# Optimization experiments

Measured on AMD Instinct MI355X. Metric: run time of the kernel, lower is better.

Reference implementation:

```python
import jax, jax.numpy as jnp
import numpy as np

B, T, H, E, D, K = 4, 4096, 2048, 8, 1024, 2

def setup_inputs() -> dict:
    key = jax.random.key(0)
    ks = jax.random.split(key, 7)
    x  = jax.random.normal(ks[0], (B, T, H), dtype=jnp.float32)
    Wr = jax.random.normal(ks[1], (H, E), dtype=jnp.float32) * (1.0 / np.sqrt(H))
    br = jnp.zeros((E,), dtype=jnp.float32)
    We = jax.random.normal(ks[2], (E, H, D), dtype=jnp.float32) * (1.0 / np.sqrt(H))
    be = jnp.zeros((E, D), dtype=jnp.float32)
    Wc = jax.random.normal(ks[3], (D, H), dtype=jnp.float32) * (1.0 / np.sqrt(D))
    bc = jnp.zeros((H,), dtype=jnp.float32)
    return {"x": x, "Wr": Wr, "br": br, "We": We, "be": be, "Wc": Wc, "bc": bc}

def reference(x, Wr, br, We, be, Wc, bc):
    # Router: [B,T,H] @ [H,E] -> [B,T,E]
    router_logits = jnp.einsum('bth,he->bte', x, Wr) + br
    scores = jax.nn.softmax(router_logits, axis=-1)
    # top-k over experts (sorted descending, like torch.topk)
    topk_scores, topk_idx = jax.lax.top_k(scores, K)  # [B,T,K]
    # Dense all-expert linear: [B,T,E,D]
    expert_outs = jnp.einsum('bth,ehd->bted', x, We) + be
    # Gather the chosen experts per token: [B,T,K,D]
    gather_idx = jnp.broadcast_to(topk_idx[..., None], (B, T, K, D))
    chosen = jnp.take_along_axis(expert_outs, gather_idx, axis=2)
    # Weighted sum over top-k: [B,T,D]
    weighted = jnp.sum(chosen * topk_scores[..., None], axis=2)
    # Combine: [B,T,D] @ [D,H] -> [B,T,H]
    return jnp.einsum('btd,dh->bth', weighted, Wc) + bc
```

## Files before the change

kernel.cpp:

```cpp
#include <hip/hip_runtime.h>
#include <hip/hip_bf16.h>

typedef float f32x4 __attribute__((ext_vector_type(4)));
typedef short bf16x8 __attribute__((ext_vector_type(8)));

#define M_NT 16
#define M_OFF 17
#define M_TBL 32
#define MAX_TILES 264
#define NCHUNK 1024

__device__ __forceinline__ void gload16(const void* g, void* l) {
  __builtin_amdgcn_global_load_lds(
      (const __attribute__((address_space(1))) void*)g,
      (__attribute__((address_space(3))) void*)l, 16, 0, 0);
}

__device__ __forceinline__ float bf2f(unsigned short u) {
  union { unsigned int i; float f; } v; v.i = ((unsigned int)u) << 16; return v.f;
}
__device__ __forceinline__ unsigned short f2bf(float f) {
  __hip_bfloat16 h = __float2bfloat16(f);
  return __builtin_bit_cast(unsigned short, h);
}

__global__ void transpose_cvt(const float* __restrict__ src,
                              unsigned short* __restrict__ dst, int R, int C) {
  __shared__ float tile[32][33];
  int b = blockIdx.z;
  int c0 = blockIdx.x * 32, r0 = blockIdx.y * 32;
  src += (size_t)b * R * C;
  dst += (size_t)b * R * C;
  int tx = threadIdx.x, ty = threadIdx.y;
#pragma unroll
  for (int i = 0; i < 32; i += 8)
    tile[ty + i][tx] = src[(size_t)(r0 + ty + i) * C + c0 + tx];
  __syncthreads();
#pragma unroll
  for (int i = 0; i < 32; i += 8)
    dst[(size_t)(c0 + ty + i) * R + r0 + tx] = f2bf(tile[tx][ty + i]);
}

__global__ __launch_bounds__(256) void router_kernel(
    const float* __restrict__ x, const float* __restrict__ Wr,
    const float* __restrict__ br, unsigned short* __restrict__ xbf,
    float* __restrict__ scores, int* __restrict__ idx,
    int* __restrict__ blk_hist) {
  __shared__ int cnt[8];
  int tid = threadIdx.x, lane = tid & 63, w = tid >> 6;
  if (tid < 8) cnt[tid] = 0;
  __syncthreads();
  int t0 = blockIdx.x * 16 + w * 4;
  const float* xr = x + (size_t)t0 * 2048;
  unsigned short* xo = xbf + (size_t)t0 * 2048;
  float acc[4][8] = {};
#pragma unroll
  for (int j = 0; j < 8; ++j) {
    int h0 = j * 256 + lane * 4;
    float4 xv[4];
#pragma unroll
    for (int t = 0; t < 4; ++t) xv[t] = *(const float4*)(xr + (size_t)t * 2048 + h0);
#pragma unroll
    for (int t = 0; t < 4; ++t) {
      ushort4 p;
      p.x = f2bf(xv[t].x); p.y = f2bf(xv[t].y);
      p.z = f2bf(xv[t].z); p.w = f2bf(xv[t].w);
      *(ushort4*)(xo + (size_t)t * 2048 + h0) = p;
    }
    const float4* wp = (const float4*)(Wr + (size_t)h0 * 8);
#pragma unroll
    for (int c = 0; c < 4; ++c) {
      float4 w0 = wp[2 * c], w1 = wp[2 * c + 1];
      float xc0 = (c == 0) ? xv[0].x : (c == 1) ? xv[0].y : (c == 2) ? xv[0].z : xv[0].w;
      float xc1 = (c == 0) ? xv[1].x : (c == 1) ? xv[1].y : (c == 2) ? xv[1].z : xv[1].w;
      float xc2 = (c == 0) ? xv[2].x : (c == 1) ? xv[2].y : (c == 2) ? xv[2].z : xv[2].w;
      float xc3 = (c == 0) ? xv[3].x : (c == 1) ? xv[3].y : (c == 2) ? xv[3].z : xv[3].w;
      acc[0][0] += xc0 * w0.x; acc[0][1] += xc0 * w0.y; acc[0][2] += xc0 * w0.z; acc[0][3] += xc0 * w0.w;
      acc[0][4] += xc0 * w1.x; acc[0][5] += xc0 * w1.y; acc[0][6] += xc0 * w1.z; acc[0][7] += xc0 * w1.w;
      acc[1][0] += xc1 * w0.x; acc[1][1] += xc1 * w0.y; acc[1][2] += xc1 * w0.z; acc[1][3] += xc1 * w0.w;
      acc[1][4] += xc1 * w1.x; acc[1][5] += xc1 * w1.y; acc[1][6] += xc1 * w1.z; acc[1][7] += xc1 * w1.w;
      acc[2][0] += xc2 * w0.x; acc[2][1] += xc2 * w0.y; acc[2][2] += xc2 * w0.z; acc[2][3] += xc2 * w0.w;
      acc[2][4] += xc2 * w1.x; acc[2][5] += xc2 * w1.y; acc[2][6] += xc2 * w1.z; acc[2][7] += xc2 * w1.w;
      acc[3][0] += xc3 * w0.x; acc[3][1] += xc3 * w0.y; acc[3][2] += xc3 * w0.z; acc[3][3] += xc3 * w0.w;
      acc[3][4] += xc3 * w1.x; acc[3][5] += xc3 * w1.y; acc[3][6] += xc3 * w1.z; acc[3][7] += xc3 * w1.w;
    }
  }
#pragma unroll
  for (int t = 0; t < 4; ++t)
#pragma unroll
    for (int e = 0; e < 8; ++e)
#pragma unroll
      for (int off = 32; off > 0; off >>= 1)
        acc[t][e] += __shfl_xor(acc[t][e], off);
  if (lane < 4) {
    int t = t0 + lane;
    float l[8];
#pragma unroll
    for (int e = 0; e < 8; ++e) {
      float v = (lane == 0) ? acc[0][e] : (lane == 1) ? acc[1][e]
              : (lane == 2) ? acc[2][e] : acc[3][e];
      l[e] = v + br[e];
    }
    float mx = l[0];
#pragma unroll
    for (int e = 1; e < 8; ++e) mx = fmaxf(mx, l[e]);
    float se = 0.f;
#pragma unroll
    for (int e = 0; e < 8; ++e) se += __expf(l[e] - mx);
    float inv = 1.f / se;
    int e1 = 0; float b1 = l[0];
#pragma unroll
    for (int e = 1; e < 8; ++e) if (l[e] > b1) { b1 = l[e]; e1 = e; }
    int e2 = -1; float b2 = -1e30f;
#pragma unroll
    for (int e = 0; e < 8; ++e) if (e != e1 && l[e] > b2) { b2 = l[e]; e2 = e; }
    idx[2 * t] = e1; idx[2 * t + 1] = e2;
    scores[2 * t] = __expf(b1 - mx) * inv;
    scores[2 * t + 1] = __expf(b2 - mx) * inv;
    atomicAdd(&cnt[e1], 1);
    atomicAdd(&cnt[e2], 1);
  }
  __syncthreads();
  if (tid < 8) blk_hist[blockIdx.x * 8 + tid] = cnt[tid];
}

__global__ __launch_bounds__(512) void scan_kernel(
    const int* __restrict__ blk_hist, int* __restrict__ chunk_base,
    int* __restrict__ meta, int* __restrict__ rowlist) {
  __shared__ int stot[8], soff[8];
  int tid = threadIdx.x, lane = tid & 63, e = tid >> 6;
  int running = 0;
  for (int g = 0; g < NCHUNK / 64; ++g) {
    int c = g * 64 + lane;
    int v = blk_hist[c * 8 + e];
    int orig = v;
#pragma unroll
    for (int off = 1; off < 64; off <<= 1) {
      int n = __shfl_up(v, off);
      if (lane >= off) v += n;
    }
    chunk_base[c * 8 + e] = running + v - orig;
    running += __shfl(v, 63);
  }
  if (lane == 0) stot[e] = running;
  __syncthreads();
  if (tid == 0) {
    int off = 0, nt = 0;
    int4* tbl = (int4*)(meta + M_TBL);
    for (int ee = 0; ee < 8; ++ee) {
      int c = stot[ee];
      meta[M_OFF + ee] = off; soff[ee] = off;
      int tiles = (c + 127) >> 7;
      for (int t = 0; t < tiles; ++t)
        tbl[nt++] = make_int4(ee, off + t * 128, min(128, c - t * 128), 0);
      off += tiles << 7;
    }
    meta[M_NT] = nt;
  }
  __syncthreads();
  for (int ee = 0; ee < 8; ++ee) {
    int c = stot[ee], end = ((c + 127) >> 7) << 7;
    for (int i = c + tid; i < end; i += 512) rowlist[soff[ee] + i] = 0;
  }
}

__global__ void scatter_kernel(const int* __restrict__ idx,
                               const int* __restrict__ chunk_base,
                               const int* __restrict__ meta,
                               int* __restrict__ rowlist) {
  int c = blockIdx.x, lane = threadIdx.x;
  int entry = c * 32 + lane;
  int e = (lane < 32) ? idx[entry] : -1;
#pragma unroll
  for (int ee = 0; ee < 8; ++ee) {
    unsigned long long m = __ballot(e == ee);
    if (e == ee) {
      int rank = __popcll(m & ((1ull << lane) - 1));
      rowlist[meta[M_OFF + ee] + chunk_base[c * 8 + ee] + rank] = entry;
    }
  }
}

__global__ __launch_bounds__(256) void expert_gemm(
    const unsigned short* __restrict__ xbf,
    const unsigned short* __restrict__ WeT,
    const float* __restrict__ be,
    const float* __restrict__ scores,
    const int* __restrict__ rowlist,
    const int* __restrict__ meta,
    unsigned short* __restrict__ z) {
  __shared__ short lA[128 * 32];
  __shared__ short lB[128 * 32];
  __shared__ int lrows[128];
  if ((int)blockIdx.y >= meta[M_NT]) return;
  int4 tt = ((const int4*)(meta + M_TBL))[blockIdx.y];
  int e = tt.x, base = tt.y, valid = tt.z;
  int n0 = blockIdx.x * 128;
  int tid = threadIdx.x, lane = tid & 63, w = tid >> 6;
  if (tid < 128) lrows[tid] = rowlist[base + tid];
  __syncthreads();
  int ch0 = 2 * w, ch1 = ch0 + 1;
  int sub = lane >> 2, colb = (lane & 3) * 8;
  int ra0 = lrows[ch0 * 16 + sub] >> 1;
  int ra1 = lrows[ch1 * 16 + sub] >> 1;
  const unsigned short* sA0 = xbf + (size_t)ra0 * 2048 + colb;
  const unsigned short* sA1 = xbf + (size_t)ra1 * 2048 + colb;
  const unsigned short* Bb = WeT + (size_t)e * 1024 * 2048;
  const unsigned short* sB0 = Bb + (size_t)(n0 + ch0 * 16 + sub) * 2048 + colb;
  const unsigned short* sB1 = Bb + (size_t)(n0 + ch1 * 16 + sub) * 2048 + colb;
  f32x4 acc[4][4] = {};
  int wr = (w >> 1) * 64, wc = (w & 1) * 64;
  int fl = lane & 15, q = lane >> 4;
  for (int k0 = 0; k0 < 2048; k0 += 32) {
    __syncthreads();
    gload16(sA0, lA + ch0 * 512);
    gload16(sA1, lA + ch1 * 512);
    gload16(sB0, lB + ch0 * 512);
    gload16(sB1, lB + ch1 * 512);
    sA0 += 32; sA1 += 32; sB0 += 32; sB1 += 32;
    __syncthreads();
    bf16x8 a[4], b[4];
#pragma unroll
    for (int i = 0; i < 4; ++i) a[i] = *(const bf16x8*)(lA + (wr + i * 16 + fl) * 32 + q * 8);
#pragma unroll
    for (int i = 0; i < 4; ++i) b[i] = *(const bf16x8*)(lB + (wc + i * 16 + fl) * 32 + q * 8);
#pragma unroll
    for (int mi = 0; mi < 4; ++mi)
#pragma unroll
      for (int ni = 0; ni < 4; ++ni)
        acc[mi][ni] = __builtin_amdgcn_mfma_f32_16x16x32_bf16(a[mi], b[ni], acc[mi][ni], 0, 0, 0);
  }
  float bev[4];
#pragma unroll
  for (int ni = 0; ni < 4; ++ni) bev[ni] = be[e * 1024 + n0 + wc + ni * 16 + fl];
#pragma unroll
  for (int mi = 0; mi < 4; ++mi)
#pragma unroll
    for (int r = 0; r < 4; ++r) {
      int row = wr + mi * 16 + q * 4 + r;
      if (row < valid) {
        int entry = lrows[row];
        float s = scores[entry];
        unsigned short* zr = z + (size_t)entry * 1024 + n0 + wc;
#pragma unroll
        for (int ni = 0; ni < 4; ++ni)
          zr[ni * 16 + fl] = f2bf((acc[mi][ni][r] + bev[ni]) * s);
      }
    }
}

__global__ void wsum_kernel(const unsigned short* __restrict__ z,
                            unsigned short* __restrict__ y) {
  size_t i = ((size_t)blockIdx.x * 256 + threadIdx.x) * 8;
  size_t t = i >> 10, d = i & 1023;
  int4 za = *(const int4*)(z + (t * 2) * 1024 + d);
  int4 zb = *(const int4*)(z + (t * 2 + 1) * 1024 + d);
  int4 r;
  const unsigned short* pa = (const unsigned short*)&za;
  const unsigned short* pb = (const unsigned short*)&zb;
  unsigned short* pr = (unsigned short*)&r;
#pragma unroll
  for (int j = 0; j < 8; ++j) pr[j] = f2bf(bf2f(pa[j]) + bf2f(pb[j]));
  *(int4*)(y + i) = r;
}

__global__ __launch_bounds__(256) void combine_gemm(
    const unsigned short* __restrict__ y,
    const unsigned short* __restrict__ WcT,
    const float* __restrict__ bc,
    float* __restrict__ out) {
  __shared__ short lA[128 * 32];
  __shared__ short lB[128 * 32];
  int tid = threadIdx.x, lane = tid & 63, w = tid >> 6;
  int m0 = blockIdx.y * 128, n0 = blockIdx.x * 128;
  int ch0 = 2 * w, ch1 = ch0 + 1;
  int sub = lane >> 2, colb = (lane & 3) * 8;
  const unsigned short* sA0 = y + (size_t)(m0 + ch0 * 16 + sub) * 1024 + colb;
  const unsigned short* sA1 = y + (size_t)(m0 + ch1 * 16 + sub) * 1024 + colb;
  const unsigned short* sB0 = WcT + (size_t)(n0 + ch0 * 16 + sub) * 1024 + colb;
  const unsigned short* sB1 = WcT + (size_t)(n0 + ch1 * 16 + sub) * 1024 + colb;
  f32x4 acc[4][4] = {};
  int wr = (w >> 1) * 64, wc = (w & 1) * 64;
  int fl = lane & 15, q = lane >> 4;
  for (int k0 = 0; k0 < 1024; k0 += 32) {
    __syncthreads();
    gload16(sA0, lA + ch0 * 512);
    gload16(sA1, lA + ch1 * 512);
    gload16(sB0, lB + ch0 * 512);
    gload16(sB1, lB + ch1 * 512);
    sA0 += 32; sA1 += 32; sB0 += 32; sB1 += 32;
    __syncthreads();
    bf16x8 a[4], b[4];
#pragma unroll
    for (int i = 0; i < 4; ++i) a[i] = *(const bf16x8*)(lA + (wr + i * 16 + fl) * 32 + q * 8);
#pragma unroll
    for (int i = 0; i < 4; ++i) b[i] = *(const bf16x8*)(lB + (wc + i * 16 + fl) * 32 + q * 8);
#pragma unroll
    for (int mi = 0; mi < 4; ++mi)
#pragma unroll
      for (int ni = 0; ni < 4; ++ni)
        acc[mi][ni] = __builtin_amdgcn_mfma_f32_16x16x32_bf16(a[mi], b[ni], acc[mi][ni], 0, 0, 0);
  }
  float bcv[4];
#pragma unroll
  for (int ni = 0; ni < 4; ++ni) bcv[ni] = bc[n0 + wc + ni * 16 + fl];
#pragma unroll
  for (int mi = 0; mi < 4; ++mi)
#pragma unroll
    for (int r = 0; r < 4; ++r) {
      int row = m0 + wr + mi * 16 + q * 4 + r;
      float* orow = out + (size_t)row * 2048 + n0 + wc;
#pragma unroll
      for (int ni = 0; ni < 4; ++ni) orow[ni * 16 + fl] = acc[mi][ni][r] + bcv[ni];
    }
}

extern "C" void kernel_launch(void* const* d_in, const int* in_sizes, int n_in,
                              void* d_out, int out_size, void* d_ws, size_t ws_size,
                              hipStream_t stream) {
  const float* x  = (const float*)d_in[0];
  const float* Wr = (const float*)d_in[1];
  const float* br = (const float*)d_in[2];
  const float* We = (const float*)d_in[3];
  const float* be = (const float*)d_in[4];
  const float* Wc = (const float*)d_in[5];
  const float* bc = (const float*)d_in[6];
  float* out = (float*)d_out;

  char* ws = (char*)d_ws;
  size_t o = 0;
  auto alloc = [&](size_t b) {
    char* p = ws + o;
    o = (o + b + 255) & ~(size_t)255;
    return p;
  };
  unsigned short* xbf = (unsigned short*)alloc(16384UL * 2048 * 2);
  unsigned short* WeT = (unsigned short*)alloc(8UL * 1024 * 2048 * 2);
  unsigned short* WcT = (unsigned short*)alloc(2048UL * 1024 * 2);
  unsigned short* z   = (unsigned short*)alloc(32768UL * 1024 * 2);
  unsigned short* yw  = (unsigned short*)alloc(16384UL * 1024 * 2);
  float* scores = (float*)alloc(32768UL * 4);
  int* idx      = (int*)alloc(32768UL * 4);
  int* rowlist  = (int*)alloc(33792UL * 4);
  int* meta     = (int*)alloc(8192);
  int* blk_hist = (int*)alloc(NCHUNK * 8 * 4);
  int* chunk_base = (int*)alloc(NCHUNK * 8 * 4);
  (void)ws_size; (void)in_sizes; (void)n_in; (void)out_size;

  hipLaunchKernelGGL(transpose_cvt, dim3(32, 64, 8), dim3(32, 8), 0, stream, We, WeT, 2048, 1024);
  hipLaunchKernelGGL(transpose_cvt, dim3(64, 32, 1), dim3(32, 8), 0, stream, Wc, WcT, 1024, 2048);
  hipLaunchKernelGGL(router_kernel, dim3(NCHUNK), dim3(256), 0, stream, x, Wr, br, xbf, scores, idx, blk_hist);
  hipLaunchKernelGGL(scan_kernel, dim3(1), dim3(512), 0, stream, blk_hist, chunk_base, meta, rowlist);
  hipLaunchKernelGGL(scatter_kernel, dim3(NCHUNK), dim3(64), 0, stream, idx, chunk_base, meta, rowlist);
  hipLaunchKernelGGL(expert_gemm, dim3(8, MAX_TILES), dim3(256), 0, stream,
                     xbf, WeT, be, scores, rowlist, meta, z);
  hipLaunchKernelGGL(wsum_kernel, dim3(8192), dim3(256), 0, stream, z, yw);
  hipLaunchKernelGGL(combine_gemm, dim3(16, 128), dim3(256), 0, stream, yw, WcT, bc, out);
}
```

Measured before the change: 433.0 us.

## Use 256x256 double-buffered swizzled LDS tiles for expert and combine GEMMs

Both GEMMs move from 128x128 tiles with a 32-wide K step and a load-then-sync loop to 256x256 tiles run by 512-thread blocks. Each K step is now 64 wide, with XOR-swizzled LDS layout and two LDS buffers: the next tile is fetched asynchronously while the current one is used, and waits are coordinated with explicit vmcnt counts. Block indices are remapped to group work for better cache locality, and the router scan now pads each expert to 256 rows instead of 128. The intent is more data reuse per LDS load and overlap of memory with MFMA work. The tradeoff is heavy register pressure from 128 accumulator floats per thread under a two-blocks-per-CU launch bound, and 128KB of shared memory per block, which limits occupancy.

```diff
diff --git a/kernel.cpp b/kernel.cpp
--- a/kernel.cpp
+++ b/kernel.cpp
@@ -7,7 +7,7 @@
 #define M_NT 16
 #define M_OFF 17
 #define M_TBL 32
-#define MAX_TILES 264
+#define MAX_TILES 136
 #define NCHUNK 1024
 
 __device__ __forceinline__ void gload16(const void* g, void* l) {
@@ -150,16 +150,16 @@
     for (int ee = 0; ee < 8; ++ee) {
       int c = stot[ee];
       meta[M_OFF + ee] = off; soff[ee] = off;
-      int tiles = (c + 127) >> 7;
+      int tiles = (c + 255) >> 8;
       for (int t = 0; t < tiles; ++t)
-        tbl[nt++] = make_int4(ee, off + t * 128, min(128, c - t * 128), 0);
-      off += tiles << 7;
+        tbl[nt++] = make_int4(ee, off + t * 256, min(256, c - t * 256), 0);
+      off += tiles << 8;
     }
     meta[M_NT] = nt;
   }
   __syncthreads();
   for (int ee = 0; ee < 8; ++ee) {
-    int c = stot[ee], end = ((c + 127) >> 7) << 7;
+    int c = stot[ee], end = ((c + 255) >> 8) << 8;
     for (int i = c + tid; i < end; i += 512) rowlist[soff[ee] + i] = 0;
   }
 }
@@ -181,7 +181,8 @@
   }
 }
 
-__global__ __launch_bounds__(256) void expert_gemm(
+
+__global__ __launch_bounds__(512, 2) void expert_gemm(
     const unsigned short* __restrict__ xbf,
     const unsigned short* __restrict__ WeT,
     const float* __restrict__ be,
@@ -189,64 +190,216 @@
     const int* __restrict__ rowlist,
     const int* __restrict__ meta,
     unsigned short* __restrict__ z) {
-  __shared__ short lA[128 * 32];
-  __shared__ short lB[128 * 32];
-  __shared__ int lrows[128];
-  if ((int)blockIdx.y >= meta[M_NT]) return;
-  int4 tt = ((const int4*)(meta + M_TBL))[blockIdx.y];
+  __shared__ char smem[131072];
+  __shared__ int lrows[256];
+  int nt = meta[M_NT];
+  int flat = blockIdx.y * 4 + blockIdx.x;
+  int work = (flat & 7) * 68 + (flat >> 3);
+  int tileid = work >> 2, nb = work & 3;
+  if (tileid >= nt) return;
+  int4 tt = ((const int4*)(meta + M_TBL))[tileid];
   int e = tt.x, base = tt.y, valid = tt.z;
-  int n0 = blockIdx.x * 128;
+  int n0 = nb * 256;
   int tid = threadIdx.x, lane = tid & 63, w = tid >> 6;
-  if (tid < 128) lrows[tid] = rowlist[base + tid];
-  __syncthreads();
-  int ch0 = 2 * w, ch1 = ch0 + 1;
-  int sub = lane >> 2, colb = (lane & 3) * 8;
-  int ra0 = lrows[ch0 * 16 + sub] >> 1;
-  int ra1 = lrows[ch1 * 16 + sub] >> 1;
-  const unsigned short* sA0 = xbf + (size_t)ra0 * 2048 + colb;
-  const unsigned short* sA1 = xbf + (size_t)ra1 * 2048 + colb;
-  const unsigned short* Bb = WeT + (size_t)e * 1024 * 2048;
-  const unsigned short* sB0 = Bb + (size_t)(n0 + ch0 * 16 + sub) * 2048 + colb;
-  const unsigned short* sB1 = Bb + (size_t)(n0 + ch1 * 16 + sub) * 2048 + colb;
-  f32x4 acc[4][4] = {};
-  int wr = (w >> 1) * 64, wc = (w & 1) * 64;
+  if (tid < 256) lrows[tid] = rowlist[base + tid];
+  __syncthreads();
+  int rsub = lane >> 3;
+  int slot = ((lane & 7) ^ rsub) * 16;
+  const char* pa[4]; const char* pb[4];
+#pragma unroll
+  for (int j = 0; j < 4; ++j) {
+    int r = w * 32 + j * 8 + rsub;
+    int tok = lrows[r] >> 1;
+    pa[j] = (const char*)(xbf + (size_t)tok * 2048) + slot;
+    pb[j] = (const char*)WeT + ((size_t)e * 1024 + n0 + r) * 4096 + slot;
+  }
+#pragma unroll
+  for (int t2 = 0; t2 < 2; ++t2) {
+    char* da = smem + t2 * 32768 + w * 4096;
+    char* db = smem + 65536 + t2 * 32768 + w * 4096;
+#pragma unroll
+    for (int j = 0; j < 4; ++j) { gload16(pa[j], da + j * 1024); pa[j] += 128; }
+#pragma unroll
+    for (int j = 0; j < 4; ++j) { gload16(pb[j], db + j * 1024); pb[j] += 128; }
+  }
+  __builtin_amdgcn_sched_barrier(0);
+  f32x4 acc[8][4] = {};
+  int wm = w >> 2, wn = w & 3;
   int fl = lane & 15, q = lane >> 4;
-  for (int k0 = 0; k0 < 2048; k0 += 32) {
-    __syncthreads();
-    gload16(sA0, lA + ch0 * 512);
-    gload16(sA1, lA + ch1 * 512);
-    gload16(sB0, lB + ch0 * 512);
-    gload16(sB1, lB + ch1 * 512);
-    sA0 += 32; sA1 += 32; sB0 += 32; sB1 += 32;
-    __syncthreads();
-    bf16x8 a[4], b[4];
-#pragma unroll
-    for (int i = 0; i < 4; ++i) a[i] = *(const bf16x8*)(lA + (wr + i * 16 + fl) * 32 + q * 8);
-#pragma unroll
-    for (int i = 0; i < 4; ++i) b[i] = *(const bf16x8*)(lB + (wc + i * 16 + fl) * 32 + q * 8);
-#pragma unroll
-    for (int mi = 0; mi < 4; ++mi)
-#pragma unroll
-      for (int ni = 0; ni < 4; ++ni)
-        acc[mi][ni] = __builtin_amdgcn_mfma_f32_16x16x32_bf16(a[mi], b[ni], acc[mi][ni], 0, 0, 0);
+  int swz = (fl & 7) << 4;
+  const int NT2 = 32;
+  for (int t = 0; t < NT2; ++t) {
+    if (t + 1 < NT2) { asm volatile("s_waitcnt vmcnt(8)" ::: "memory"); }
+    else             { asm volatile("s_waitcnt vmcnt(0)" ::: "memory"); }
+    __builtin_amdgcn_sched_barrier(0);
+    __builtin_amdgcn_s_barrier();
+    __builtin_amdgcn_sched_barrier(0);
+    const char* Ab = smem + (t & 1) * 32768;
+    const char* Bb = smem + 65536 + (t & 1) * 32768;
+#pragma unroll
+    for (int mh = 0; mh < 2; ++mh)
+#pragma unroll
+      for (int nh = 0; nh < 2; ++nh) {
+        bf16x8 av[4][2], bv[2][2];
+#pragma unroll
+        for (int m = 0; m < 4; ++m)
+#pragma unroll
+          for (int kk = 0; kk < 2; ++kk) {
+            int row = wm * 128 + mh * 64 + m * 16 + fl;
+            av[m][kk] = *(const bf16x8*)(Ab + row * 128 + ((kk * 64 + q * 16) ^ swz));
+          }
+#pragma unroll
+        for (int n = 0; n < 2; ++n)
+#pragma unroll
+          for (int kk = 0; kk < 2; ++kk) {
+            int row = wn * 64 + nh * 32 + n * 16 + fl;
+            bv[n][kk] = *(const bf16x8*)(Bb + row * 128 + ((kk * 64 + q * 16) ^ swz));
+          }
+        __builtin_amdgcn_s_setprio(1);
+#pragma unroll
+        for (int m = 0; m < 4; ++m)
+#pragma unroll
+          for (int n = 0; n < 2; ++n)
+#pragma unroll
+            for (int kk = 0; kk < 2; ++kk)
+              acc[mh * 4 + m][nh * 2 + n] = __builtin_amdgcn_mfma_f32_16x16x32_bf16(
+                  av[m][kk], bv[n][kk], acc[mh * 4 + m][nh * 2 + n], 0, 0, 0);
+        __builtin_amdgcn_s_setprio(0);
+      }
+    __builtin_amdgcn_sched_barrier(0);
+    __builtin_amdgcn_s_barrier();
+    __builtin_amdgcn_sched_barrier(0);
+    if (t + 2 < NT2) {
+      char* da = smem + (t & 1) * 32768 + w * 4096;
+      char* db = smem + 65536 + (t & 1) * 32768 + w * 4096;
+#pragma unroll
+      for (int j = 0; j < 4; ++j) { gload16(pa[j], da + j * 1024); pa[j] += 128; }
+#pragma unroll
+      for (int j = 0; j < 4; ++j) { gload16(pb[j], db + j * 1024); pb[j] += 128; }
+    }
   }
   float bev[4];
 #pragma unroll
-  for (int ni = 0; ni < 4; ++ni) bev[ni] = be[e * 1024 + n0 + wc + ni * 16 + fl];
-#pragma unroll
-  for (int mi = 0; mi < 4; ++mi)
+  for (int nc = 0; nc < 4; ++nc)
+    bev[nc] = be[e * 1024 + n0 + wn * 64 + (nc >> 1) * 32 + (nc & 1) * 16 + fl];
+#pragma unroll
+  for (int mi = 0; mi < 8; ++mi) {
+    int rowbase = wm * 128 + (mi >> 2) * 64 + (mi & 3) * 16 + q * 4;
 #pragma unroll
     for (int r = 0; r < 4; ++r) {
-      int row = wr + mi * 16 + q * 4 + r;
+      int row = rowbase + r;
       if (row < valid) {
         int entry = lrows[row];
         float s = scores[entry];
-        unsigned short* zr = z + (size_t)entry * 1024 + n0 + wc;
-#pragma unroll
-        for (int ni = 0; ni < 4; ++ni)
-          zr[ni * 16 + fl] = f2bf((acc[mi][ni][r] + bev[ni]) * s);
+        unsigned short* zr = z + (size_t)entry * 1024 + n0 + wn * 64 + fl;
+#pragma unroll
+        for (int nc = 0; nc < 4; ++nc)
+          zr[(nc >> 1) * 32 + (nc & 1) * 16] = f2bf((acc[mi][nc][r] + bev[nc]) * s);
       }
     }
+  }
+}
+
+__global__ __launch_bounds__(512, 2) void combine_gemm(
+    const unsigned short* __restrict__ y,
+    const unsigned short* __restrict__ WcT,
+    const float* __restrict__ bc,
+    float* __restrict__ out) {
+  __shared__ char smem[131072];
+  int flat = blockIdx.y * 8 + blockIdx.x;
+  int work = (flat & 7) * 64 + (flat >> 3);
+  int mtile = work >> 3, nb = work & 7;
+  int m0 = mtile * 256, n0 = nb * 256;
+  int tid = threadIdx.x, lane = tid & 63, w = tid >> 6;
+  int rsub = lane >> 3;
+  int slot = ((lane & 7) ^ rsub) * 16;
+  const char* pa[4]; const char* pb[4];
+#pragma unroll
+  for (int j = 0; j < 4; ++j) {
+    int r = w * 32 + j * 8 + rsub;
+    pa[j] = (const char*)y + (size_t)(m0 + r) * 2048 + slot;
+    pb[j] = (const char*)WcT + (size_t)(n0 + r) * 2048 + slot;
+  }
+#pragma unroll
+  for (int t2 = 0; t2 < 2; ++t2) {
+    char* da = smem + t2 * 32768 + w * 4096;
+    char* db = smem + 65536 + t2 * 32768 + w * 4096;
+#pragma unroll
+    for (int j = 0; j < 4; ++j) { gload16(pa[j], da + j * 1024); pa[j] += 128; }
+#pragma unroll
+    for (int j = 0; j < 4; ++j) { gload16(pb[j], db + j * 1024); pb[j] += 128; }
+  }
+  __builtin_amdgcn_sched_barrier(0);
+  f32x4 acc[8][4] = {};
+  int wm = w >> 2, wn = w & 3;
+  int fl = lane & 15, q = lane >> 4;
+  int swz = (fl & 7) << 4;
+  const int NT2 = 16;
+  for (int t = 0; t < NT2; ++t) {
+    if (t + 1 < NT2) { asm volatile("s_waitcnt vmcnt(8)" ::: "memory"); }
+    else             { asm volatile("s_waitcnt vmcnt(0)" ::: "memory"); }
+    __builtin_amdgcn_sched_barrier(0);
+    __builtin_amdgcn_s_barrier();
+    __builtin_amdgcn_sched_barrier(0);
+    const char* Ab = smem + (t & 1) * 32768;
+    const char* Bb = smem + 65536 + (t & 1) * 32768;
+#pragma unroll
+    for (int mh = 0; mh < 2; ++mh)
+#pragma unroll
+      for (int nh = 0; nh < 2; ++nh) {
+        bf16x8 av[4][2], bv[2][2];
+#pragma unroll
+        for (int m = 0; m < 4; ++m)
+#pragma unroll
+          for (int kk = 0; kk < 2; ++kk) {
+            int row = wm * 128 + mh * 64 + m * 16 + fl;
+            av[m][kk] = *(const bf16x8*)(Ab + row * 128 + ((kk * 64 + q * 16) ^ swz));
+          }
+#pragma unroll
+        for (int n = 0; n < 2; ++n)
+#pragma unroll
+          for (int kk = 0; kk < 2; ++kk) {
+            int row = wn * 64 + nh * 32 + n * 16 + fl;
+            bv[n][kk] = *(const bf16x8*)(Bb + row * 128 + ((kk * 64 + q * 16) ^ swz));
+          }
+        __builtin_amdgcn_s_setprio(1);
+#pragma unroll
+        for (int m = 0; m < 4; ++m)
+#pragma unroll
+          for (int n = 0; n < 2; ++n)
+#pragma unroll
+            for (int kk = 0; kk < 2; ++kk)
+              acc[mh * 4 + m][nh * 2 + n] = __builtin_amdgcn_mfma_f32_16x16x32_bf16(
+                  av[m][kk], bv[n][kk], acc[mh * 4 + m][nh * 2 + n], 0, 0, 0);
+        __builtin_amdgcn_s_setprio(0);
+      }
+    __builtin_amdgcn_sched_barrier(0);
+    __builtin_amdgcn_s_barrier();
+    __builtin_amdgcn_sched_barrier(0);
+    if (t + 2 < NT2) {
+      char* da = smem + (t & 1) * 32768 + w * 4096;
+      char* db = smem + 65536 + (t & 1) * 32768 + w * 4096;
+#pragma unroll
+      for (int j = 0; j < 4; ++j) { gload16(pa[j], da + j * 1024); pa[j] += 128; }
+#pragma unroll
+      for (int j = 0; j < 4; ++j) { gload16(pb[j], db + j * 1024); pb[j] += 128; }
+    }
+  }
+  float bcv[4];
+#pragma unroll
+  for (int nc = 0; nc < 4; ++nc)
+    bcv[nc] = bc[n0 + wn * 64 + (nc >> 1) * 32 + (nc & 1) * 16 + fl];
+#pragma unroll
+  for (int mi = 0; mi < 8; ++mi) {
+    int rowbase = m0 + wm * 128 + (mi >> 2) * 64 + (mi & 3) * 16 + q * 4;
+#pragma unroll
+    for (int r = 0; r < 4; ++r) {
+      float* orow = out + (size_t)(rowbase + r) * 2048 + n0 + wn * 64 + fl;
+#pragma unroll
+      for (int nc = 0; nc < 4; ++nc)
+        orow[(nc >> 1) * 32 + (nc & 1) * 16] = acc[mi][nc][r] + bcv[nc];
+    }
+  }
 }
 
 __global__ void wsum_kernel(const unsigned short* __restrict__ z,
@@ -262,57 +415,6 @@
 #pragma unroll
   for (int j = 0; j < 8; ++j) pr[j] = f2bf(bf2f(pa[j]) + bf2f(pb[j]));
   *(int4*)(y + i) = r;
-}
-
-__global__ __launch_bounds__(256) void combine_gemm(
-    const unsigned short* __restrict__ y,
-    const unsigned short* __restrict__ WcT,
-    const float* __restrict__ bc,
-    float* __restrict__ out) {
-  __shared__ short lA[128 * 32];
-  __shared__ short lB[128 * 32];
-  int tid = threadIdx.x, lane = tid & 63, w = tid >> 6;
-  int m0 = blockIdx.y * 128, n0 = blockIdx.x * 128;
-  int ch0 = 2 * w, ch1 = ch0 + 1;
-  int sub = lane >> 2, colb = (lane & 3) * 8;
-  const unsigned short* sA0 = y + (size_t)(m0 + ch0 * 16 + sub) * 1024 + colb;
-  const unsigned short* sA1 = y + (size_t)(m0 + ch1 * 16 + sub) * 1024 + colb;
-  const unsigned short* sB0 = WcT + (size_t)(n0 + ch0 * 16 + sub) * 1024 + colb;
-  const unsigned short* sB1 = WcT + (size_t)(n0 + ch1 * 16 + sub) * 1024 + colb;
-  f32x4 acc[4][4] = {};
-  int wr = (w >> 1) * 64, wc = (w & 1) * 64;
-  int fl = lane & 15, q = lane >> 4;
-  for (int k0 = 0; k0 < 1024; k0 += 32) {
-    __syncthreads();
-    gload16(sA0, lA + ch0 * 512);
-    gload16(sA1, lA + ch1 * 512);
-    gload16(sB0, lB + ch0 * 512);
-    gload16(sB1, lB + ch1 * 512);
-    sA0 += 32; sA1 += 32; sB0 += 32; sB1 += 32;
-    __syncthreads();
-    bf16x8 a[4], b[4];
-#pragma unroll
-    for (int i = 0; i < 4; ++i) a[i] = *(const bf16x8*)(lA + (wr + i * 16 + fl) * 32 + q * 8);
-#pragma unroll
-    for (int i = 0; i < 4; ++i) b[i] = *(const bf16x8*)(lB + (wc + i * 16 + fl) * 32 + q * 8);
-#pragma unroll
-    for (int mi = 0; mi < 4; ++mi)
-#pragma unroll
-      for (int ni = 0; ni < 4; ++ni)
-        acc[mi][ni] = __builtin_amdgcn_mfma_f32_16x16x32_bf16(a[mi], b[ni], acc[mi][ni], 0, 0, 0);
-  }
-  float bcv[4];
-#pragma unroll
-  for (int ni = 0; ni < 4; ++ni) bcv[ni] = bc[n0 + wc + ni * 16 + fl];
-#pragma unroll
-  for (int mi = 0; mi < 4; ++mi)
-#pragma unroll
-    for (int r = 0; r < 4; ++r) {
-      int row = m0 + wr + mi * 16 + q * 4 + r;
-      float* orow = out + (size_t)row * 2048 + n0 + wc;
-#pragma unroll
-      for (int ni = 0; ni < 4; ++ni) orow[ni * 16 + fl] = acc[mi][ni][r] + bcv[ni];
-    }
 }
 
 extern "C" void kernel_launch(void* const* d_in, const int* in_sizes, int n_in,
@@ -341,7 +443,7 @@
   unsigned short* yw  = (unsigned short*)alloc(16384UL * 1024 * 2);
   float* scores = (float*)alloc(32768UL * 4);
   int* idx      = (int*)alloc(32768UL * 4);
-  int* rowlist  = (int*)alloc(33792UL * 4);
+  int* rowlist  = (int*)alloc(36864UL * 4);
   int* meta     = (int*)alloc(8192);
   int* blk_hist = (int*)alloc(NCHUNK * 8 * 4);
   int* chunk_base = (int*)alloc(NCHUNK * 8 * 4);
@@ -352,8 +454,8 @@
   hipLaunchKernelGGL(router_kernel, dim3(NCHUNK), dim3(256), 0, stream, x, Wr, br, xbf, scores, idx, blk_hist);
   hipLaunchKernelGGL(scan_kernel, dim3(1), dim3(512), 0, stream, blk_hist, chunk_base, meta, rowlist);
   hipLaunchKernelGGL(scatter_kernel, dim3(NCHUNK), dim3(64), 0, stream, idx, chunk_base, meta, rowlist);
-  hipLaunchKernelGGL(expert_gemm, dim3(8, MAX_TILES), dim3(256), 0, stream,
+  hipLaunchKernelGGL(expert_gemm, dim3(4, MAX_TILES), dim3(512), 0, stream,
                      xbf, WeT, be, scores, rowlist, meta, z);
   hipLaunchKernelGGL(wsum_kernel, dim3(8192), dim3(256), 0, stream, z, yw);
-  hipLaunchKernelGGL(combine_gemm, dim3(16, 128), dim3(256), 0, stream, yw, WcT, bc, out);
-}
+  hipLaunchKernelGGL(combine_gemm, dim3(8, 64), dim3(512), 0, stream, yw, WcT, bc, out);
+}
```

After: 425.4 us. No clear change (-1.8%).

## Rewrite expert and combine GEMMs with 256x256 tiles and pipelined swizzled LDS

Applied to the files above, without the earlier changes.

Both GEMMs move from 128x128 tiles with a single 32-wide K stage and two barriers per step to 256x256 tiles with 512 threads and 64-wide K stages. The new loop double-buffers direct-to-LDS loads, uses an XOR-swizzled LDS layout, interleaves MFMA clusters with prefetches, and uses partial vmcnt waits and setprio. The routing tables are rebuilt for 256-row tiles and blocks are remapped across XCDs. This targets the exposed load latency and low arithmetic intensity of the old kernels. In exchange, the larger tiles waste more padded rows for experts with ragged token counts and raise register and LDS pressure.

```diff
diff --git a/kernel.cpp b/kernel.cpp
--- a/kernel.cpp
+++ b/kernel.cpp
@@ -7,7 +7,7 @@
 #define M_NT 16
 #define M_OFF 17
 #define M_TBL 32
-#define MAX_TILES 264
+#define MAX_TILES 136
 #define NCHUNK 1024
 
 __device__ __forceinline__ void gload16(const void* g, void* l) {
@@ -23,6 +23,10 @@
   __hip_bfloat16 h = __float2bfloat16(f);
   return __builtin_bit_cast(unsigned short, h);
 }
+
+#define CBAR() do { asm volatile("" ::: "memory"); __builtin_amdgcn_s_barrier(); asm volatile("" ::: "memory"); } while (0)
+#define VMC6() asm volatile("s_waitcnt vmcnt(6)" ::: "memory")
+#define VMC0() asm volatile("s_waitcnt vmcnt(0)" ::: "memory")
 
 __global__ void transpose_cvt(const float* __restrict__ src,
                               unsigned short* __restrict__ dst, int R, int C) {
@@ -150,16 +154,16 @@
     for (int ee = 0; ee < 8; ++ee) {
       int c = stot[ee];
       meta[M_OFF + ee] = off; soff[ee] = off;
-      int tiles = (c + 127) >> 7;
+      int tiles = (c + 255) >> 8;
       for (int t = 0; t < tiles; ++t)
-        tbl[nt++] = make_int4(ee, off + t * 128, min(128, c - t * 128), 0);
-      off += tiles << 7;
+        tbl[nt++] = make_int4(ee, off + t * 256, min(256, c - t * 256), 0);
+      off += tiles << 8;
     }
     meta[M_NT] = nt;
   }
   __syncthreads();
   for (int ee = 0; ee < 8; ++ee) {
-    int c = stot[ee], end = ((c + 127) >> 7) << 7;
+    int c = stot[ee], end = ((c + 255) >> 8) << 8;
     for (int i = c + tid; i < end; i += 512) rowlist[soff[ee] + i] = 0;
   }
 }
@@ -181,7 +185,70 @@
   }
 }
 
-__global__ __launch_bounds__(256) void expert_gemm(
+
+#define STG(P0, P1, KOFF, D) { gload16((P0) + (KOFF), (D)); gload16((P1) + (KOFF), (D) + 8192); }
+
+#define RD_A(OFF) do { _Pragma("unroll") for (int m = 0; m < 4; ++m) { \
+  av[m][0] = *(const bf16x8*)(aP0 + (OFF) + m * 2048); \
+  av[m][1] = *(const bf16x8*)(aP1 + (OFF) + m * 2048); } } while (0)
+
+#define RD_B(BV, OFF) do { _Pragma("unroll") for (int n = 0; n < 2; ++n) { \
+  BV[n][0] = *(const bf16x8*)(bP0 + (OFF) + n * 2048); \
+  BV[n][1] = *(const bf16x8*)(bP1 + (OFF) + n * 2048); } } while (0)
+
+#define CLUSTER(MO, NO, BV) do { \
+  __builtin_amdgcn_s_setprio(1); \
+  _Pragma("unroll") for (int kk = 0; kk < 2; ++kk) \
+  _Pragma("unroll") for (int m = 0; m < 4; ++m) \
+  _Pragma("unroll") for (int n = 0; n < 2; ++n) \
+    acc[(MO) + m][(NO) + n] = __builtin_amdgcn_mfma_f32_16x16x32_bf16( \
+        av[m][kk], BV[n][kk], acc[(MO) + m][(NO) + n], 0, 0, 0); \
+  __builtin_amdgcn_s_setprio(0); \
+} while (0)
+
+#define GEMM_ITER(PF) \
+     \
+    RD_A(0); RD_B(bv0, 0); \
+    STG(paG[1][0], paG[1][1], 128, dA + 32768 + 16384);             \
+    CBAR(); CLUSTER(0, 0, bv0); CBAR(); \
+    RD_B(bv1, 4096); \
+    if (PF) STG(pbG[0][0], pbG[0][1], 256, dB);                     \
+    CBAR(); CLUSTER(0, 2, bv1); CBAR(); \
+    RD_A(8192); \
+    if (PF) STG(pbG[1][0], pbG[1][1], 256, dB + 16384);             \
+    CBAR(); CLUSTER(4, 0, bv0); CBAR(); \
+    if (PF) STG(paG[0][0], paG[0][1], 256, dA);                     \
+    CBAR(); CLUSTER(4, 2, bv1); \
+    if (PF) { VMC6(); } else { VMC0(); } \
+    CBAR(); \
+     \
+    RD_A(32768); RD_B(bv0, 32768); \
+    if (PF) STG(paG[1][0], paG[1][1], 256, dA + 16384);             \
+    CBAR(); CLUSTER(0, 0, bv0); CBAR(); \
+    RD_B(bv1, 32768 + 4096); \
+    if (PF) STG(pbG[0][0], pbG[0][1], 384, dB + 32768);             \
+    CBAR(); CLUSTER(0, 2, bv1); CBAR(); \
+    RD_A(32768 + 8192); \
+    if (PF) STG(pbG[1][0], pbG[1][1], 384, dB + 32768 + 16384);     \
+    CBAR(); CLUSTER(4, 0, bv0); CBAR(); \
+    if (PF) STG(paG[0][0], paG[0][1], 384, dA + 32768);             \
+    CBAR(); CLUSTER(4, 2, bv1); \
+    if (PF) { VMC6(); } else { VMC0(); } \
+    CBAR(); \
+    _Pragma("unroll") for (int h_ = 0; h_ < 2; ++h_) \
+    _Pragma("unroll") for (int j_ = 0; j_ < 2; ++j_) { paG[h_][j_] += 256; pbG[h_][j_] += 256; }
+
+#define GEMM_PROLOGUE() \
+    STG(pbG[0][0], pbG[0][1], 0, dB); \
+    STG(pbG[1][0], pbG[1][1], 0, dB + 16384); \
+    STG(paG[0][0], paG[0][1], 0, dA); \
+    STG(paG[1][0], paG[1][1], 0, dA + 16384); \
+    STG(pbG[0][0], pbG[0][1], 128, dB + 32768); \
+    STG(pbG[1][0], pbG[1][1], 128, dB + 32768 + 16384); \
+    STG(paG[0][0], paG[0][1], 128, dA + 32768); \
+    VMC6(); CBAR();
+
+__global__ __launch_bounds__(512, 2) void expert_gemm(
     const unsigned short* __restrict__ xbf,
     const unsigned short* __restrict__ WeT,
     const float* __restrict__ be,
@@ -189,64 +256,127 @@
     const int* __restrict__ rowlist,
     const int* __restrict__ meta,
     unsigned short* __restrict__ z) {
-  __shared__ short lA[128 * 32];
-  __shared__ short lB[128 * 32];
-  __shared__ int lrows[128];
-  if ((int)blockIdx.y >= meta[M_NT]) return;
-  int4 tt = ((const int4*)(meta + M_TBL))[blockIdx.y];
+  __shared__ char smem[131072];
+  __shared__ int lrows[256];
+  int nt = meta[M_NT];
+  int flat = blockIdx.y * 4 + blockIdx.x;
+  int work = (flat & 7) * 68 + (flat >> 3);
+  int tileid = work >> 2, nb = work & 3;
+  if (tileid >= nt) return;
+  int4 tt = ((const int4*)(meta + M_TBL))[tileid];
   int e = tt.x, base = tt.y, valid = tt.z;
-  int n0 = blockIdx.x * 128;
+  int n0 = nb * 256;
   int tid = threadIdx.x, lane = tid & 63, w = tid >> 6;
-  if (tid < 128) lrows[tid] = rowlist[base + tid];
-  __syncthreads();
-  int ch0 = 2 * w, ch1 = ch0 + 1;
-  int sub = lane >> 2, colb = (lane & 3) * 8;
-  int ra0 = lrows[ch0 * 16 + sub] >> 1;
-  int ra1 = lrows[ch1 * 16 + sub] >> 1;
-  const unsigned short* sA0 = xbf + (size_t)ra0 * 2048 + colb;
-  const unsigned short* sA1 = xbf + (size_t)ra1 * 2048 + colb;
-  const unsigned short* Bb = WeT + (size_t)e * 1024 * 2048;
-  const unsigned short* sB0 = Bb + (size_t)(n0 + ch0 * 16 + sub) * 2048 + colb;
-  const unsigned short* sB1 = Bb + (size_t)(n0 + ch1 * 16 + sub) * 2048 + colb;
-  f32x4 acc[4][4] = {};
-  int wr = (w >> 1) * 64, wc = (w & 1) * 64;
+  if (tid < 256) lrows[tid] = rowlist[base + tid];
+  __syncthreads();
+  int wm = w >> 2, wn = w & 3;
   int fl = lane & 15, q = lane >> 4;
-  for (int k0 = 0; k0 < 2048; k0 += 32) {
-    __syncthreads();
-    gload16(sA0, lA + ch0 * 512);
-    gload16(sA1, lA + ch1 * 512);
-    gload16(sB0, lB + ch0 * 512);
-    gload16(sB1, lB + ch1 * 512);
-    sA0 += 32; sA1 += 32; sB0 += 32; sB1 += 32;
-    __syncthreads();
-    bf16x8 a[4], b[4];
-#pragma unroll
-    for (int i = 0; i < 4; ++i) a[i] = *(const bf16x8*)(lA + (wr + i * 16 + fl) * 32 + q * 8);
-#pragma unroll
-    for (int i = 0; i < 4; ++i) b[i] = *(const bf16x8*)(lB + (wc + i * 16 + fl) * 32 + q * 8);
-#pragma unroll
-    for (int mi = 0; mi < 4; ++mi)
-#pragma unroll
-      for (int ni = 0; ni < 4; ++ni)
-        acc[mi][ni] = __builtin_amdgcn_mfma_f32_16x16x32_bf16(a[mi], b[ni], acc[mi][ni], 0, 0, 0);
+  int rowb = tid >> 3;
+  int dstB = rowb * 128 + (tid & 7) * 16;
+  int s16 = ((tid & 7) ^ (rowb & 7)) * 16;
+  const char* paG[2][2]; const char* pbG[2][2];
+#pragma unroll
+  for (int h = 0; h < 2; ++h)
+#pragma unroll
+    for (int j = 0; j < 2; ++j) {
+      int R = h * 128 + j * 64 + rowb;
+      paG[h][j] = (const char*)xbf + (size_t)(lrows[R] >> 1) * 4096 + s16;
+      pbG[h][j] = (const char*)WeT + ((size_t)e * 1024 + n0 + R) * 4096 + s16;
+    }
+  char* dA = smem + 65536 + dstB;
+  char* dB = smem + dstB;
+  int sw16 = (fl & 7) << 4;
+  int axk0 = (q * 16) ^ sw16, axk1 = (64 + q * 16) ^ sw16;
+  const char* aP0 = smem + 65536 + (wm * 128 + fl) * 128 + axk0;
+  const char* aP1 = smem + 65536 + (wm * 128 + fl) * 128 + axk1;
+  const char* bP0 = smem + (wn * 64 + fl) * 128 + axk0;
+  const char* bP1 = smem + (wn * 64 + fl) * 128 + axk1;
+  GEMM_PROLOGUE();
+  f32x4 acc[8][4] = {};
+  bf16x8 av[4][2], bv0[2][2], bv1[2][2];
+  const int NT = 32;
+  for (int t2 = 0; t2 < NT; t2 += 2) {
+    const bool pf = (t2 + 2) < NT;
+    GEMM_ITER(pf);
   }
   float bev[4];
 #pragma unroll
-  for (int ni = 0; ni < 4; ++ni) bev[ni] = be[e * 1024 + n0 + wc + ni * 16 + fl];
-#pragma unroll
-  for (int mi = 0; mi < 4; ++mi)
+  for (int nc = 0; nc < 4; ++nc)
+    bev[nc] = be[e * 1024 + n0 + wn * 64 + (nc >> 1) * 32 + (nc & 1) * 16 + fl];
+#pragma unroll
+  for (int mi = 0; mi < 8; ++mi) {
+    int rowbase = wm * 128 + (mi >> 2) * 64 + (mi & 3) * 16 + q * 4;
 #pragma unroll
     for (int r = 0; r < 4; ++r) {
-      int row = wr + mi * 16 + q * 4 + r;
+      int row = rowbase + r;
       if (row < valid) {
         int entry = lrows[row];
         float s = scores[entry];
-        unsigned short* zr = z + (size_t)entry * 1024 + n0 + wc;
-#pragma unroll
-        for (int ni = 0; ni < 4; ++ni)
-          zr[ni * 16 + fl] = f2bf((acc[mi][ni][r] + bev[ni]) * s);
+        unsigned short* zr = z + (size_t)entry * 1024 + n0 + wn * 64 + fl;
+#pragma unroll
+        for (int nc = 0; nc < 4; ++nc)
+          zr[(nc >> 1) * 32 + (nc & 1) * 16] = f2bf((acc[mi][nc][r] + bev[nc]) * s);
       }
     }
+  }
+}
+
+__global__ __launch_bounds__(512, 2) void combine_gemm(
+    const unsigned short* __restrict__ y,
+    const unsigned short* __restrict__ WcT,
+    const float* __restrict__ bc,
+    float* __restrict__ out) {
+  __shared__ char smem[131072];
+  int flat = blockIdx.y * 8 + blockIdx.x;
+  int work = (flat & 7) * 64 + (flat >> 3);
+  int mtile = work >> 3, nb = work & 7;
+  int m0 = mtile * 256, n0 = nb * 256;
+  int tid = threadIdx.x, lane = tid & 63, w = tid >> 6;
+  int wm = w >> 2, wn = w & 3;
+  int fl = lane & 15, q = lane >> 4;
+  int rowb = tid >> 3;
+  int dstB = rowb * 128 + (tid & 7) * 16;
+  int s16 = ((tid & 7) ^ (rowb & 7)) * 16;
+  const char* paG[2][2]; const char* pbG[2][2];
+#pragma unroll
+  for (int h = 0; h < 2; ++h)
+#pragma unroll
+    for (int j = 0; j < 2; ++j) {
+      int R = h * 128 + j * 64 + rowb;
+      paG[h][j] = (const char*)y + (size_t)(m0 + R) * 2048 + s16;
+      pbG[h][j] = (const char*)WcT + (size_t)(n0 + R) * 2048 + s16;
+    }
+  char* dA = smem + 65536 + dstB;
+  char* dB = smem + dstB;
+  int sw16 = (fl & 7) << 4;
+  int axk0 = (q * 16) ^ sw16, axk1 = (64 + q * 16) ^ sw16;
+  const char* aP0 = smem + 65536 + (wm * 128 + fl) * 128 + axk0;
+  const char* aP1 = smem + 65536 + (wm * 128 + fl) * 128 + axk1;
+  const char* bP0 = smem + (wn * 64 + fl) * 128 + axk0;
+  const char* bP1 = smem + (wn * 64 + fl) * 128 + axk1;
+  GEMM_PROLOGUE();
+  f32x4 acc[8][4] = {};
+  bf16x8 av[4][2], bv0[2][2], bv1[2][2];
+  const int NT = 16;
+  for (int t2 = 0; t2 < NT; t2 += 2) {
+    const bool pf = (t2 + 2) < NT;
+    GEMM_ITER(pf);
+  }
+  float bcv[4];
+#pragma unroll
+  for (int nc = 0; nc < 4; ++nc)
+    bcv[nc] = bc[n0 + wn * 64 + (nc >> 1) * 32 + (nc & 1) * 16 + fl];
+#pragma unroll
+  for (int mi = 0; mi < 8; ++mi) {
+    int rowbase = m0 + wm * 128 + (mi >> 2) * 64 + (mi & 3) * 16 + q * 4;
+#pragma unroll
+    for (int r = 0; r < 4; ++r) {
+      float* orow = out + (size_t)(rowbase + r) * 2048 + n0 + wn * 64 + fl;
+#pragma unroll
+      for (int nc = 0; nc < 4; ++nc)
+        orow[(nc >> 1) * 32 + (nc & 1) * 16] = acc[mi][nc][r] + bcv[nc];
+    }
+  }
 }
 
 __global__ void wsum_kernel(const unsigned short* __restrict__ z,
@@ -262,57 +392,6 @@
 #pragma unroll
   for (int j = 0; j < 8; ++j) pr[j] = f2bf(bf2f(pa[j]) + bf2f(pb[j]));
   *(int4*)(y + i) = r;
-}
-
-__global__ __launch_bounds__(256) void combine_gemm(
-    const unsigned short* __restrict__ y,
-    const unsigned short* __restrict__ WcT,
-    const float* __restrict__ bc,
-    float* __restrict__ out) {
-  __shared__ short lA[128 * 32];
-  __shared__ short lB[128 * 32];
-  int tid = threadIdx.x, lane = tid & 63, w = tid >> 6;
-  int m0 = blockIdx.y * 128, n0 = blockIdx.x * 128;
-  int ch0 = 2 * w, ch1 = ch0 + 1;
-  int sub = lane >> 2, colb = (lane & 3) * 8;
-  const unsigned short* sA0 = y + (size_t)(m0 + ch0 * 16 + sub) * 1024 + colb;
-  const unsigned short* sA1 = y + (size_t)(m0 + ch1 * 16 + sub) * 1024 + colb;
-  const unsigned short* sB0 = WcT + (size_t)(n0 + ch0 * 16 + sub) * 1024 + colb;
-  const unsigned short* sB1 = WcT + (size_t)(n0 + ch1 * 16 + sub) * 1024 + colb;
-  f32x4 acc[4][4] = {};
-  int wr = (w >> 1) * 64, wc = (w & 1) * 64;
-  int fl = lane & 15, q = lane >> 4;
-  for (int k0 = 0; k0 < 1024; k0 += 32) {
-    __syncthreads();
-    gload16(sA0, lA + ch0 * 512);
-    gload16(sA1, lA + ch1 * 512);
-    gload16(sB0, lB + ch0 * 512);
-    gload16(sB1, lB + ch1 * 512);
-    sA0 += 32; sA1 += 32; sB0 += 32; sB1 += 32;
-    __syncthreads();
-    bf16x8 a[4], b[4];
-#pragma unroll
-    for (int i = 0; i < 4; ++i) a[i] = *(const bf16x8*)(lA + (wr + i * 16 + fl) * 32 + q * 8);
-#pragma unroll
-    for (int i = 0; i < 4; ++i) b[i] = *(const bf16x8*)(lB + (wc + i * 16 + fl) * 32 + q * 8);
-#pragma unroll
-    for (int mi = 0; mi < 4; ++mi)
-#pragma unroll
-      for (int ni = 0; ni < 4; ++ni)
-        acc[mi][ni] = __builtin_amdgcn_mfma_f32_16x16x32_bf16(a[mi], b[ni], acc[mi][ni], 0, 0, 0);
-  }
-  float bcv[4];
-#pragma unroll
-  for (int ni = 0; ni < 4; ++ni) bcv[ni] = bc[n0 + wc + ni * 16 + fl];
-#pragma unroll
-  for (int mi = 0; mi < 4; ++mi)
-#pragma unroll
-    for (int r = 0; r < 4; ++r) {
-      int row = m0 + wr + mi * 16 + q * 4 + r;
-      float* orow = out + (size_t)row * 2048 + n0 + wc;
-#pragma unroll
-      for (int ni = 0; ni < 4; ++ni) orow[ni * 16 + fl] = acc[mi][ni][r] + bcv[ni];
-    }
 }
 
 extern "C" void kernel_launch(void* const* d_in, const int* in_sizes, int n_in,
@@ -341,7 +420,7 @@
   unsigned short* yw  = (unsigned short*)alloc(16384UL * 1024 * 2);
   float* scores = (float*)alloc(32768UL * 4);
   int* idx      = (int*)alloc(32768UL * 4);
-  int* rowlist  = (int*)alloc(33792UL * 4);
+  int* rowlist  = (int*)alloc(36864UL * 4);
   int* meta     = (int*)alloc(8192);
   int* blk_hist = (int*)alloc(NCHUNK * 8 * 4);
   int* chunk_base = (int*)alloc(NCHUNK * 8 * 4);
@@ -352,8 +431,8 @@
   hipLaunchKernelGGL(router_kernel, dim3(NCHUNK), dim3(256), 0, stream, x, Wr, br, xbf, scores, idx, blk_hist);
   hipLaunchKernelGGL(scan_kernel, dim3(1), dim3(512), 0, stream, blk_hist, chunk_base, meta, rowlist);
   hipLaunchKernelGGL(scatter_kernel, dim3(NCHUNK), dim3(64), 0, stream, idx, chunk_base, meta, rowlist);
-  hipLaunchKernelGGL(expert_gemm, dim3(8, MAX_TILES), dim3(256), 0, stream,
+  hipLaunchKernelGGL(expert_gemm, dim3(4, MAX_TILES), dim3(512), 0, stream,
                      xbf, WeT, be, scores, rowlist, meta, z);
   hipLaunchKernelGGL(wsum_kernel, dim3(8192), dim3(256), 0, stream, z, yw);
-  hipLaunchKernelGGL(combine_gemm, dim3(16, 128), dim3(256), 0, stream, yw, WcT, bc, out);
-}
+  hipLaunchKernelGGL(combine_gemm, dim3(8, 64), dim3(512), 0, stream, yw, WcT, bc, out);
+}
```

Measured after the change: 383.9 us. -11.3%, faster.
